# Performance work log

Measured on AMD Instinct MI355X. Metric: run time of the kernel, lower is better.

The kernel has to match this reference:

```python
import jax, jax.numpy as jnp
import numpy as np

BN_EPS = 1e-5


def setup_inputs() -> dict:
    key = jax.random.key(0)
    k1, k2 = jax.random.split(key, 2)
    N_out, K, Cin, Cout = 65536, 8, 256, 512
    N_in = N_out * K
    data = jax.random.normal(k1, (N_in, Cin), dtype=jnp.float32)
    # Kaiming-ish scale for the conv weight [K*Cin, Cout]
    weight = jax.random.normal(k2, (K * Cin, Cout), dtype=jnp.float32) * (1.0 / np.sqrt(K * Cin))
    bias = jnp.zeros((Cout,), dtype=jnp.float32)
    gamma = jnp.ones((Cout,), dtype=jnp.float32)
    beta = jnp.zeros((Cout,), dtype=jnp.float32)
    # Full-octree stride-2 child indices: output node i gathers children 8i..8i+7
    neigh = jnp.arange(N_in, dtype=jnp.int64).reshape(N_out, K)
    return {"data": data, "weight": weight, "bias": bias,
            "gamma": gamma, "beta": beta, "neigh": neigh}


def reference(data, weight, bias, gamma, beta, neigh):
    # OctreeConv (kernel 2x2x2, stride 2, nempty): gather 8 children per output
    # node, then a single GEMM with weight [8*Cin, Cout].
    N_out, K = neigh.shape
    Cin = data.shape[1]
    feat = data[neigh.reshape(-1)].reshape(N_out, K * Cin)  # [N_out, 8*Cin]
    out = feat @ weight + bias                              # [N_out, Cout]
    # BatchNorm1d, training mode: biased batch stats over the node dim.
    mean = jnp.mean(out, axis=0)
    var = jnp.mean(jnp.square(out), axis=0) - jnp.square(mean)
    out = (out - mean) * jax.lax.rsqrt(var + BN_EPS) * gamma + beta
    return out
```

## Files before the change

### kernel.cpp

```cpp
#include <hip/hip_runtime.h>
#include <hip/hip_bf16.h>

typedef __attribute__((ext_vector_type(8))) short bf16x8;
typedef __attribute__((ext_vector_type(4))) float f32x4;

#define N_OUT 65536
#define CIN   256
#define COUT  512
#define BM    128
#define BK    32
#define NKS   64

__device__ __forceinline__ unsigned short f2bf(float f) {
  union { __hip_bfloat16 h; unsigned short u; } c;
  c.h = __float2bfloat16(f);
  return c.u;
}

__device__ __forceinline__ bf16x8 pack8(f32x4 a, f32x4 b) {
  unsigned short u[8];
  u[0] = f2bf(a.x); u[1] = f2bf(a.y); u[2] = f2bf(a.z); u[3] = f2bf(a.w);
  u[4] = f2bf(b.x); u[5] = f2bf(b.y); u[6] = f2bf(b.z); u[7] = f2bf(b.w);
  return *reinterpret_cast<bf16x8*>(u);
}

__device__ __forceinline__ void gload_lds16f(const float* g, float* l) {
  __builtin_amdgcn_global_load_lds(
      (const __attribute__((address_space(1))) void*)g,
      (__attribute__((address_space(3))) void*)l, 16, 0, 0);
}
__device__ __forceinline__ void gload_lds16u(const unsigned short* g, unsigned short* l) {
  __builtin_amdgcn_global_load_lds(
      (const __attribute__((address_space(1))) void*)g,
      (__attribute__((address_space(3))) void*)l, 16, 0, 0);
}

__global__ void wprep_kernel(const float* __restrict__ W, unsigned short* __restrict__ Wt) {
  int idx = blockIdx.x * blockDim.x + threadIdx.x;
  if (idx >= 64 * 4 * COUT) return;
  int n  = idx & (COUT - 1);
  int s  = (idx >> 9) & 3;
  int kb = idx >> 11;
  unsigned short tmp[8];
#pragma unroll
  for (int w = 0; w < 8; ++w)
    tmp[w] = f2bf(W[(size_t)(kb * 32 + s * 8 + w) * COUT + n]);
  *reinterpret_cast<bf16x8*>(Wt + ((size_t)kb * 16384 + s * 4096 + n * 8)) =
      *reinterpret_cast<bf16x8*>(tmp);
}

__global__ __launch_bounds__(512, 2) void gemm_kernel(
    const float* __restrict__ data,
    const int*   __restrict__ neigh,
    const unsigned short* __restrict__ Wt,
    float* __restrict__ out,
    float* __restrict__ psum,
    float* __restrict__ psq)
{
  __shared__ union {
    struct {
      float          a[3][BM * BK];
      unsigned short b[3][BK * COUT];
    } r;
    float st[4][COUT];
  } sm;
  __shared__ unsigned int offs[BM * 8];

  const int tid = threadIdx.x;
  const int l   = tid & 63;
  const int w   = tid >> 6;
  const int wr  = w >> 2;
  const int wc  = w & 3;
  const int lg  = l >> 4;
  const int lm  = l & 15;
  const int m0  = blockIdx.x * BM;

  f32x4 acc[4][8];
#pragma unroll
  for (int i = 0; i < 4; ++i)
#pragma unroll
    for (int j = 0; j < 8; ++j) acc[i][j] = (f32x4){0.f, 0.f, 0.f, 0.f};

  bf16x8 af[4], bf[8];

  for (int e = tid; e < BM * 8; e += 512)
    offs[e] = ((unsigned)neigh[(size_t)m0 * 8 + e]) << 8;
  __syncthreads();

#define AISSUE(t_, buf_) do { \
    const int cn_ = (t_) >> 3; \
    const int k0_ = ((t_) & 7) * BK; \
    _Pragma("unroll") \
    for (int q_ = 0; q_ < 2; ++q_) { \
      int row_ = w * 16 + q_ * 8 + (l >> 3); \
      unsigned off_ = offs[row_ * 8 + cn_]; \
      const float* src_ = data + off_ + k0_ + (((l & 7) ^ ((l >> 3) & 7)) << 2); \
      gload_lds16f(src_, &sm.r.a[buf_][(w * 16 + q_ * 8) * BK]); \
    } \
  } while (0)

#define BISSUE(t_, buf_) do { \
    const unsigned short* bs_ = Wt + (size_t)(t_) * 16384; \
    _Pragma("unroll") \
    for (int p_ = 0; p_ < 4; ++p_) \
      gload_lds16u(bs_ + (w * 4 + p_) * 512 + l * 8, &sm.r.b[buf_][(w * 4 + p_) * 512]); \
  } while (0)

#define LOAD_AF(buf_) do { \
    _Pragma("unroll") \
    for (int mi_ = 0; mi_ < 4; ++mi_) { \
      int R_ = wr * 64 + mi_ * 16 + lm; \
      const f32x4* b_ = reinterpret_cast<const f32x4*>(&sm.r.a[buf_][R_ * BK]); \
      f32x4 x0_ = b_[(2 * lg)     ^ (R_ & 7)]; \
      f32x4 x1_ = b_[(2 * lg + 1) ^ (R_ & 7)]; \
      af[mi_] = pack8(x0_, x1_); \
    } \
  } while (0)

#define LOAD_BF(buf_) do { \
    _Pragma("unroll") \
    for (int ni_ = 0; ni_ < 8; ++ni_) \
      bf[ni_] = *reinterpret_cast<const bf16x8*>( \
          &sm.r.b[buf_][lg * 4096 + (wc * 128 + lm + ni_ * 16) * 8]); \
  } while (0)

#define DO_MFMA() do { \
    _Pragma("unroll") \
    for (int mi_ = 0; mi_ < 4; ++mi_) \
      _Pragma("unroll") \
      for (int ni_ = 0; ni_ < 8; ++ni_) \
        acc[mi_][ni_] = __builtin_amdgcn_mfma_f32_16x16x32_bf16(af[mi_], bf[ni_], acc[mi_][ni_], 0, 0, 0); \
  } while (0)

  BISSUE(0, 0); AISSUE(0, 0);
  BISSUE(1, 1); AISSUE(1, 1);

  int bufc = 0, bufp = 2;
#pragma unroll 1
  for (int t = 0; t < NKS - 2; ++t) {
    BISSUE(t + 2, bufp);
    AISSUE(t + 2, bufp);
    asm volatile("s_waitcnt vmcnt(12)" ::: "memory");
    __builtin_amdgcn_s_barrier();
    LOAD_AF(bufc);
    LOAD_BF(bufc);
    DO_MFMA();
    __builtin_amdgcn_s_barrier();
    bufc = (bufc == 2) ? 0 : bufc + 1;
    bufp = (bufp == 2) ? 0 : bufp + 1;
  }
  asm volatile("s_waitcnt vmcnt(6)" ::: "memory");
  __builtin_amdgcn_s_barrier();
  LOAD_AF(bufc); LOAD_BF(bufc); DO_MFMA();
  bufc = (bufc == 2) ? 0 : bufc + 1;
  asm volatile("s_waitcnt vmcnt(0)" ::: "memory");
  __builtin_amdgcn_s_barrier();
  LOAD_AF(bufc); LOAD_BF(bufc); DO_MFMA();

#pragma unroll
  for (int mi = 0; mi < 4; ++mi) {
#pragma unroll
    for (int r = 0; r < 4; ++r) {
      size_t row = (size_t)(m0 + wr * 64 + mi * 16 + lg * 4 + r);
      float* op = out + row * COUT + wc * 128 + lm;
#pragma unroll
      for (int ni = 0; ni < 8; ++ni) op[ni * 16] = acc[mi][ni][r];
    }
  }

  __syncthreads();
#pragma unroll
  for (int ni = 0; ni < 8; ++ni) {
    float s1 = 0.f, s2 = 0.f;
#pragma unroll
    for (int mi = 0; mi < 4; ++mi)
#pragma unroll
      for (int r = 0; r < 4; ++r) { float v = acc[mi][ni][r]; s1 += v; s2 += v * v; }
    s1 += __shfl_xor(s1, 16, 64); s1 += __shfl_xor(s1, 32, 64);
    s2 += __shfl_xor(s2, 16, 64); s2 += __shfl_xor(s2, 32, 64);
    if (l < 16) {
      sm.st[wr][wc * 128 + ni * 16 + l]     = s1;
      sm.st[2 + wr][wc * 128 + ni * 16 + l] = s2;
    }
  }
  __syncthreads();
  {
    float S = sm.st[0][tid] + sm.st[1][tid];
    float Q = sm.st[2][tid] + sm.st[3][tid];
    psum[(size_t)blockIdx.x * COUT + tid] = S;
    psq [(size_t)blockIdx.x * COUT + tid] = Q;
  }
#undef AISSUE
#undef BISSUE
#undef LOAD_AF
#undef LOAD_BF
#undef DO_MFMA
}

__global__ void reduce1_kernel(const float* __restrict__ psum, const float* __restrict__ psq,
                               float* __restrict__ p2) {
  int c = threadIdx.x, b = blockIdx.x;
  float s = 0.f, q = 0.f;
#pragma unroll
  for (int j = 0; j < 8; ++j) {
    s += psum[(size_t)(b * 8 + j) * COUT + c];
    q += psq [(size_t)(b * 8 + j) * COUT + c];
  }
  p2[b * 1024 + c] = s;
  p2[b * 1024 + 512 + c] = q;
}

__global__ void reduce2_kernel(const float* __restrict__ p2,
                               const float* __restrict__ gamma,
                               const float* __restrict__ beta,
                               float* __restrict__ scsh) {
  int c = threadIdx.x;
  float s = 0.f, q = 0.f;
  for (int b = 0; b < 64; ++b) { s += p2[b * 1024 + c]; q += p2[b * 1024 + 512 + c]; }
  float mean = s * (1.f / 65536.f);
  float var  = q * (1.f / 65536.f) - mean * mean;
  float rs   = rsqrtf(var + 1e-5f);
  float sc   = gamma[c] * rs;
  scsh[c] = sc;
  scsh[COUT + c] = beta[c] - mean * sc;
}

__global__ void bn_kernel(float* __restrict__ out, const float* __restrict__ scsh) {
  __shared__ float sc[COUT], sh[COUT];
  int t = threadIdx.x;
  sc[t] = scsh[t];
  sh[t] = scsh[COUT + t];
  __syncthreads();
  f32x4* o4 = reinterpret_cast<f32x4*>(out);
  const size_t total  = (size_t)N_OUT * COUT / 4;
  const size_t stride = (size_t)gridDim.x * blockDim.x;
  for (size_t i = (size_t)blockIdx.x * blockDim.x + t; i < total; i += stride) {
    f32x4 v = o4[i];
    int c = ((int)(i & 127)) * 4;
    v.x = v.x * sc[c]     + sh[c];
    v.y = v.y * sc[c + 1] + sh[c + 1];
    v.z = v.z * sc[c + 2] + sh[c + 2];
    v.w = v.w * sc[c + 3] + sh[c + 3];
    o4[i] = v;
  }
}

extern "C" void kernel_launch(void* const* d_in, const int* in_sizes, int n_in,
                              void* d_out, int out_size, void* d_ws, size_t ws_size,
                              hipStream_t stream) {
  const float* data   = (const float*)d_in[0];
  const float* weight = (const float*)d_in[1];
  const float* gamma  = (const float*)d_in[3];
  const float* beta   = (const float*)d_in[4];
  const int*   neigh  = (const int*)d_in[5];
  float* out = (float*)d_out;

  char* ws = (char*)d_ws;
  unsigned short* Wt = (unsigned short*)ws;
  float* psum = (float*)(ws + (2u << 20));
  float* psq  = (float*)(ws + (3u << 20));
  float* p2   = (float*)(ws + (4u << 20));
  float* scsh = (float*)(ws + (4u << 20) + (256u << 10));

  wprep_kernel<<<512, 256, 0, stream>>>(weight, Wt);
  gemm_kernel<<<N_OUT / BM, 512, 0, stream>>>(data, neigh, Wt, out, psum, psq);
  reduce1_kernel<<<64, 512, 0, stream>>>(psum, psq, p2);
  reduce2_kernel<<<1, 512, 0, stream>>>(p2, gamma, beta, scsh);
  bn_kernel<<<2048, 512, 0, stream>>>(out, scsh);
}
```

Baseline: 306.1 us.

## Shrink GEMM tile to 64 rows with 256 threads and double buffering

Changes the fused gather-GEMM block tile from 128 rows with 512 threads and triple buffering to 64 rows with 256 threads and double buffering. Each wave now covers 32x256 outputs, loading B fragments inside the MFMA loop. Neighbour offsets are read straight into registers instead of staged in shared memory. Also adds an s_setprio hint around the MFMAs and swizzles the block-to-row mapping for locality. The aim is more resident blocks and less LDS per block, at the cost of re-reading the B weight tile twice as often, a shallower prefetch pipeline, and more partial-stat rows to reduce.

```diff
diff --git a/kernel.cpp b/kernel.cpp
--- a/kernel.cpp
+++ b/kernel.cpp
@@ -7,7 +7,7 @@
 #define N_OUT 65536
 #define CIN   256
 #define COUT  512
-#define BM    128
+#define BM    64
 #define BK    32
 #define NKS   64
 
@@ -49,7 +49,7 @@
       *reinterpret_cast<bf16x8*>(tmp);
 }
 
-__global__ __launch_bounds__(512, 2) void gemm_kernel(
+__global__ __launch_bounds__(256, 2) void gemm_kernel(
     const float* __restrict__ data,
     const int*   __restrict__ neigh,
     const unsigned short* __restrict__ Wt,
@@ -59,142 +59,138 @@
 {
   __shared__ union {
     struct {
-      float          a[3][BM * BK];
-      unsigned short b[3][BK * COUT];
+      float          a[2][BM * BK];
+      unsigned short b[2][BK * COUT];
     } r;
     float st[4][COUT];
   } sm;
-  __shared__ unsigned int offs[BM * 8];
 
   const int tid = threadIdx.x;
   const int l   = tid & 63;
   const int w   = tid >> 6;
-  const int wr  = w >> 2;
-  const int wc  = w & 3;
+  const int wr  = w >> 1;
+  const int wc  = w & 1;
   const int lg  = l >> 4;
   const int lm  = l & 15;
-  const int m0  = blockIdx.x * BM;
-
-  f32x4 acc[4][8];
-#pragma unroll
-  for (int i = 0; i < 4; ++i)
-#pragma unroll
-    for (int j = 0; j < 8; ++j) acc[i][j] = (f32x4){0.f, 0.f, 0.f, 0.f};
-
-  bf16x8 af[4], bf[8];
-
-  for (int e = tid; e < BM * 8; e += 512)
-    offs[e] = ((unsigned)neigh[(size_t)m0 * 8 + e]) << 8;
-  __syncthreads();
-
-#define AISSUE(t_, buf_) do { \
-    const int cn_ = (t_) >> 3; \
-    const int k0_ = ((t_) & 7) * BK; \
+
+  const int bid = blockIdx.x;
+  const int m0  = ((bid & 7) * 128 + (bid >> 3)) * BM;
+
+  const int r0 = w * 16 + (l >> 3);
+
+  f32x4 acc[2][16];
+#pragma unroll
+  for (int i = 0; i < 2; ++i)
+#pragma unroll
+    for (int j = 0; j < 16; ++j) acc[i][j] = (f32x4){0.f, 0.f, 0.f, 0.f};
+
+  bf16x8 af[2];
+
+#define AISSUE(k0_, buf_, o0_, o1_) do { \
+    gload_lds16f(data + (o0_) + (k0_) + (((l & 7) ^ ((l >> 3) & 7)) << 2), \
+                 &sm.r.a[buf_][(w * 16) * BK]); \
+    gload_lds16f(data + (o1_) + (k0_) + (((l & 7) ^ ((l >> 3) & 7)) << 2), \
+                 &sm.r.a[buf_][(w * 16 + 8) * BK]); \
+  } while (0)
+
+#define BISSUE(kb_, buf_) do { \
+    const unsigned short* bs_ = Wt + (size_t)(kb_) * 16384; \
     _Pragma("unroll") \
-    for (int q_ = 0; q_ < 2; ++q_) { \
-      int row_ = w * 16 + q_ * 8 + (l >> 3); \
-      unsigned off_ = offs[row_ * 8 + cn_]; \
-      const float* src_ = data + off_ + k0_ + (((l & 7) ^ ((l >> 3) & 7)) << 2); \
-      gload_lds16f(src_, &sm.r.a[buf_][(w * 16 + q_ * 8) * BK]); \
-    } \
+    for (int p_ = 0; p_ < 8; ++p_) \
+      gload_lds16u(bs_ + (w * 8 + p_) * 512 + l * 8, \
+                   &sm.r.b[buf_][(w * 8 + p_) * 512]); \
   } while (0)
 
-#define BISSUE(t_, buf_) do { \
-    const unsigned short* bs_ = Wt + (size_t)(t_) * 16384; \
+#define COMPUTE(buf_) do { \
     _Pragma("unroll") \
-    for (int p_ = 0; p_ < 4; ++p_) \
-      gload_lds16u(bs_ + (w * 4 + p_) * 512 + l * 8, &sm.r.b[buf_][(w * 4 + p_) * 512]); \
-  } while (0)
-
-#define LOAD_AF(buf_) do { \
-    _Pragma("unroll") \
-    for (int mi_ = 0; mi_ < 4; ++mi_) { \
-      int R_ = wr * 64 + mi_ * 16 + lm; \
+    for (int mi_ = 0; mi_ < 2; ++mi_) { \
+      int R_ = wr * 32 + mi_ * 16 + lm; \
       const f32x4* b_ = reinterpret_cast<const f32x4*>(&sm.r.a[buf_][R_ * BK]); \
       f32x4 x0_ = b_[(2 * lg)     ^ (R_ & 7)]; \
       f32x4 x1_ = b_[(2 * lg + 1) ^ (R_ & 7)]; \
       af[mi_] = pack8(x0_, x1_); \
     } \
+    __builtin_amdgcn_s_setprio(1); \
+    _Pragma("unroll") \
+    for (int ni_ = 0; ni_ < 16; ++ni_) { \
+      bf16x8 bfr_ = *reinterpret_cast<const bf16x8*>( \
+          &sm.r.b[buf_][lg * 4096 + (wc * 256 + ni_ * 16 + lm) * 8]); \
+      acc[0][ni_] = __builtin_amdgcn_mfma_f32_16x16x32_bf16(af[0], bfr_, acc[0][ni_], 0, 0, 0); \
+      acc[1][ni_] = __builtin_amdgcn_mfma_f32_16x16x32_bf16(af[1], bfr_, acc[1][ni_], 0, 0, 0); \
+    } \
+    __builtin_amdgcn_s_setprio(0); \
   } while (0)
 
-#define LOAD_BF(buf_) do { \
-    _Pragma("unroll") \
-    for (int ni_ = 0; ni_ < 8; ++ni_) \
-      bf[ni_] = *reinterpret_cast<const bf16x8*>( \
-          &sm.r.b[buf_][lg * 4096 + (wc * 128 + lm + ni_ * 16) * 8]); \
-  } while (0)
-
-#define DO_MFMA() do { \
-    _Pragma("unroll") \
-    for (int mi_ = 0; mi_ < 4; ++mi_) \
-      _Pragma("unroll") \
-      for (int ni_ = 0; ni_ < 8; ++ni_) \
-        acc[mi_][ni_] = __builtin_amdgcn_mfma_f32_16x16x32_bf16(af[mi_], bf[ni_], acc[mi_][ni_], 0, 0, 0); \
-  } while (0)
-
-  BISSUE(0, 0); AISSUE(0, 0);
-  BISSUE(1, 1); AISSUE(1, 1);
-
-  int bufc = 0, bufp = 2;
+  unsigned offA0 = ((unsigned)neigh[(m0 + r0) * 8])     << 8;
+  unsigned offA1 = ((unsigned)neigh[(m0 + r0 + 8) * 8]) << 8;
+  AISSUE(0,  0, offA0, offA1); BISSUE(0, 0);
+  AISSUE(32, 1, offA0, offA1); BISSUE(1, 1);
+
 #pragma unroll 1
-  for (int t = 0; t < NKS - 2; ++t) {
-    BISSUE(t + 2, bufp);
-    AISSUE(t + 2, bufp);
-    asm volatile("s_waitcnt vmcnt(12)" ::: "memory");
-    __builtin_amdgcn_s_barrier();
-    LOAD_AF(bufc);
-    LOAD_BF(bufc);
-    DO_MFMA();
-    __builtin_amdgcn_s_barrier();
-    bufc = (bufc == 2) ? 0 : bufc + 1;
-    bufp = (bufp == 2) ? 0 : bufp + 1;
-  }
-  asm volatile("s_waitcnt vmcnt(6)" ::: "memory");
-  __builtin_amdgcn_s_barrier();
-  LOAD_AF(bufc); LOAD_BF(bufc); DO_MFMA();
-  bufc = (bufc == 2) ? 0 : bufc + 1;
-  asm volatile("s_waitcnt vmcnt(0)" ::: "memory");
-  __builtin_amdgcn_s_barrier();
-  LOAD_AF(bufc); LOAD_BF(bufc); DO_MFMA();
-
-#pragma unroll
-  for (int mi = 0; mi < 4; ++mi) {
+  for (int cn = 0; cn < 8; ++cn) {
+    const int cnn = (cn < 7) ? cn + 1 : 7;
+    unsigned offB0 = ((unsigned)neigh[(m0 + r0) * 8 + cnn])     << 8;
+    unsigned offB1 = ((unsigned)neigh[(m0 + r0 + 8) * 8 + cnn]) << 8;
+#pragma unroll
+    for (int j = 0; j < 8; ++j) {
+      if (j == 7) {
+        if (cn == 7) asm volatile("s_waitcnt vmcnt(0)" ::: "memory");
+        else         asm volatile("s_waitcnt vmcnt(10)" ::: "memory");
+      } else {
+        asm volatile("s_waitcnt vmcnt(10)" ::: "memory");
+      }
+      __builtin_amdgcn_s_barrier();
+      asm volatile("" ::: "memory");
+      COMPUTE(j & 1);
+      asm volatile("" ::: "memory");
+      __builtin_amdgcn_s_barrier();
+      if (j < 6) {
+        AISSUE(((j + 2) & 7) * BK, j & 1, offA0, offA1);
+        BISSUE(cn * 8 + j + 2, j & 1);
+      } else if (cn < 7) {
+        AISSUE(((j + 2) & 7) * BK, j & 1, offB0, offB1);
+        BISSUE(cn * 8 + j + 2, j & 1);
+      }
+    }
+    offA0 = offB0; offA1 = offB1;
+  }
+
+#pragma unroll
+  for (int mi = 0; mi < 2; ++mi) {
 #pragma unroll
     for (int r = 0; r < 4; ++r) {
-      size_t row = (size_t)(m0 + wr * 64 + mi * 16 + lg * 4 + r);
-      float* op = out + row * COUT + wc * 128 + lm;
-#pragma unroll
-      for (int ni = 0; ni < 8; ++ni) op[ni * 16] = acc[mi][ni][r];
+      size_t row = (size_t)(m0 + wr * 32 + mi * 16 + lg * 4 + r);
+      float* op = out + row * COUT + wc * 256 + lm;
+#pragma unroll
+      for (int ni = 0; ni < 16; ++ni) op[ni * 16] = acc[mi][ni][r];
     }
   }
 
   __syncthreads();
 #pragma unroll
-  for (int ni = 0; ni < 8; ++ni) {
+  for (int ni = 0; ni < 16; ++ni) {
     float s1 = 0.f, s2 = 0.f;
 #pragma unroll
-    for (int mi = 0; mi < 4; ++mi)
+    for (int mi = 0; mi < 2; ++mi)
 #pragma unroll
       for (int r = 0; r < 4; ++r) { float v = acc[mi][ni][r]; s1 += v; s2 += v * v; }
     s1 += __shfl_xor(s1, 16, 64); s1 += __shfl_xor(s1, 32, 64);
     s2 += __shfl_xor(s2, 16, 64); s2 += __shfl_xor(s2, 32, 64);
     if (l < 16) {
-      sm.st[wr][wc * 128 + ni * 16 + l]     = s1;
-      sm.st[2 + wr][wc * 128 + ni * 16 + l] = s2;
+      sm.st[wr][wc * 256 + ni * 16 + l]     = s1;
+      sm.st[2 + wr][wc * 256 + ni * 16 + l] = s2;
     }
   }
   __syncthreads();
-  {
-    float S = sm.st[0][tid] + sm.st[1][tid];
-    float Q = sm.st[2][tid] + sm.st[3][tid];
-    psum[(size_t)blockIdx.x * COUT + tid] = S;
-    psq [(size_t)blockIdx.x * COUT + tid] = Q;
+#pragma unroll
+  for (int h = 0; h < 2; ++h) {
+    int c = h * 256 + tid;
+    psum[(size_t)blockIdx.x * COUT + c] = sm.st[0][c] + sm.st[1][c];
+    psq [(size_t)blockIdx.x * COUT + c] = sm.st[2][c] + sm.st[3][c];
   }
 #undef AISSUE
 #undef BISSUE
-#undef LOAD_AF
-#undef LOAD_BF
-#undef DO_MFMA
+#undef COMPUTE
 }
 
 __global__ void reduce1_kernel(const float* __restrict__ psum, const float* __restrict__ psq,
@@ -202,9 +198,9 @@
   int c = threadIdx.x, b = blockIdx.x;
   float s = 0.f, q = 0.f;
 #pragma unroll
-  for (int j = 0; j < 8; ++j) {
-    s += psum[(size_t)(b * 8 + j) * COUT + c];
-    q += psq [(size_t)(b * 8 + j) * COUT + c];
+  for (int j = 0; j < 16; ++j) {
+    s += psum[(size_t)(b * 16 + j) * COUT + c];
+    q += psq [(size_t)(b * 16 + j) * COUT + c];
   }
   p2[b * 1024 + c] = s;
   p2[b * 1024 + 512 + c] = q;
@@ -258,12 +254,12 @@
   char* ws = (char*)d_ws;
   unsigned short* Wt = (unsigned short*)ws;
   float* psum = (float*)(ws + (2u << 20));
-  float* psq  = (float*)(ws + (3u << 20));
-  float* p2   = (float*)(ws + (4u << 20));
-  float* scsh = (float*)(ws + (4u << 20) + (256u << 10));
+  float* psq  = (float*)(ws + (4u << 20));
+  float* p2   = (float*)(ws + (6u << 20));
+  float* scsh = (float*)(ws + (6u << 20) + (256u << 10));
 
   wprep_kernel<<<512, 256, 0, stream>>>(weight, Wt);
-  gemm_kernel<<<N_OUT / BM, 512, 0, stream>>>(data, neigh, Wt, out, psum, psq);
+  gemm_kernel<<<N_OUT / BM, 256, 0, stream>>>(data, neigh, Wt, out, psum, psq);
   reduce1_kernel<<<64, 512, 0, stream>>>(psum, psq, p2);
   reduce2_kernel<<<1, 512, 0, stream>>>(p2, gamma, beta, scsh);
   bn_kernel<<<2048, 512, 0, stream>>>(out, scsh);
```

New measurement: 865.9 us. 2.83x slower.
